# Performance work log

Measured on AMD Instinct MI355X. Metric: run time of the kernel, lower is better.

The kernel has to match this reference:

```python
import jax, jax.numpy as jnp
import numpy as np

MARGIN = 1.0

def setup_inputs() -> dict:
    key = jax.random.key(0)
    k1, k2, k3 = jax.random.split(key, 3)
    B, C, D = 65536, 1000, 512
    x = jax.random.normal(k1, (B, D), dtype=jnp.float32)
    x = x / jnp.linalg.norm(x, axis=1, keepdims=True)  # docstring: ||x||2 = 1
    labels = jax.random.randint(k2, (B,), 0, C, dtype=jnp.int64)
    centers = jax.random.normal(k3, (C, D), dtype=jnp.float32)
    return {"x": x, "labels": labels, "centers": centers}

def reference(x, labels, centers):
    # l2Norm applied to the centers (module is only used when l2Norm is truthy)
    c = centers / jnp.linalg.norm(centers, axis=1, keepdims=True)  # (C, D)
    # cosine distance to every center: one batched GEMM instead of per-sample loop
    dist = 1.0 - jnp.einsum("bd,cd->bc", x, c)                      # (B, C)
    pos = jnp.take_along_axis(dist, labels[:, None], axis=1)[:, 0]  # (B,)
    # min over all classes != label: mask own class with +inf
    same = jnp.arange(c.shape[0])[None, :] == labels[:, None]       # (B, C)
    neg = jnp.min(jnp.where(same, jnp.inf, dist), axis=1)           # (B,)
    # sum of per-sample hinge losses divided by batch size == mean
    return jnp.mean(jax.nn.relu(pos + MARGIN - neg))
```

## Files before the change

### kernel.cpp

```cpp
#include <hip/hip_runtime.h>
#include <stdint.h>

typedef short v8s __attribute__((ext_vector_type(8)));
typedef short v4s __attribute__((ext_vector_type(4)));
typedef float v4f __attribute__((ext_vector_type(4)));

#define BM 256
#define BN 128
#define BK 64
#define POS_INF __builtin_inff()

typedef __attribute__((address_space(3))) unsigned int lds_uint;
typedef const __attribute__((address_space(1))) unsigned int glb_uint;

__device__ __forceinline__ void load16_lds(const void* g, void* l) {
    __builtin_amdgcn_global_load_lds((glb_uint*)g, (lds_uint*)l, 16, 0, 0);
}

__device__ __forceinline__ short f2bf(float f) {
    uint32_t u = __builtin_bit_cast(uint32_t, f);
    u += 0x7fffu + ((u >> 16) & 1u);
    return (short)(u >> 16);
}

__global__ void prep(const float* __restrict__ centers,
                     unsigned short* __restrict__ cbf,
                     int C, int D, int CP, int CB,
                     const float* __restrict__ x,
                     unsigned short* __restrict__ xbf, size_t nx,
                     int* __restrict__ cnt, int NB,
                     float* __restrict__ out) {
    const int b = blockIdx.x;
    const int t = threadIdx.x;
    if (b == 0 && t == 0) out[0] = 0.0f;
    if (b < CB) {
        const int g = b * 256 + t;
        if (g < NB) cnt[g] = 0;
        const int wave = t >> 6, lane = t & 63;
        const int row = b * 4 + wave;
        if (row >= CP) return;
        if (row >= C) {
            v4s z = {0, 0, 0, 0};
            for (int d = lane * 4; d < D; d += 256)
                *(v4s*)&cbf[(size_t)row * D + d] = z;
            return;
        }
        const float* src = centers + (size_t)row * D;
        float ss = 0.0f;
        for (int d = lane * 4; d < D; d += 256) {
            v4f f = *(const v4f*)&src[d];
            ss += f.x * f.x + f.y * f.y + f.z * f.z + f.w * f.w;
        }
        #pragma unroll
        for (int off = 32; off; off >>= 1) ss += __shfl_xor(ss, off, 64);
        const float rn = rsqrtf(ss);
        for (int d = lane * 4; d < D; d += 256) {
            v4f f = *(const v4f*)&src[d];
            v4s s;
            s.x = f2bf(f.x * rn); s.y = f2bf(f.y * rn);
            s.z = f2bf(f.z * rn); s.w = f2bf(f.w * rn);
            *(v4s*)&cbf[(size_t)row * D + d] = s;
        }
    } else {
        const size_t i = ((size_t)(b - CB) * 256 + t) * 8;
        if (i >= nx) return;
        v4f f0 = *(const v4f*)&x[i];
        v4f f1 = *(const v4f*)&x[i + 4];
        v8s s;
        s[0] = f2bf(f0.x); s[1] = f2bf(f0.y); s[2] = f2bf(f0.z); s[3] = f2bf(f0.w);
        s[4] = f2bf(f1.x); s[5] = f2bf(f1.y); s[6] = f2bf(f1.z); s[7] = f2bf(f1.w);
        *(v8s*)&xbf[i] = s;
    }
}

__global__ void __launch_bounds__(512)
gemm_fused(const unsigned short* __restrict__ xbf,
           const unsigned short* __restrict__ cbf,
           const int* __restrict__ labels,
           float* __restrict__ pos, float* __restrict__ partial,
           int* __restrict__ cnt,
           int Bt, int C, int D, int NT, float margin,
           float* __restrict__ out) {
    __shared__ short LDSbuf[(BM + BN) * BK];
    short* As = LDSbuf;
    short* Bs = LDSbuf + BM * BK;

    const int t   = threadIdx.x;
    const int bid = blockIdx.x;
    const int xcd = bid & 7;
    const int per = bid >> 3;
    const int rowblk = (per >> 3) * 8 + xcd;
    const int nt     = per & 7;
    const int row0 = rowblk * BM;
    const int n0   = nt * BN;

    const int lane = t & 63;
    const int wave = t >> 6;
    const int wm = wave >> 1;
    const int wn = wave & 1;
    const int l15 = lane & 15, q = lane >> 4;

    const int rsub = lane >> 3;
    const int csrc = (lane & 7) ^ rsub;

    int myLab = 0;
    if (t < BM) myLab = labels[row0 + t];

    v4f acc[4][4];
    #pragma unroll
    for (int i = 0; i < 4; ++i)
        #pragma unroll
        for (int j = 0; j < 4; ++j)
            acc[i][j] = (v4f){0.f, 0.f, 0.f, 0.f};

    const int KT = D / BK;
    for (int kk = 0; kk < KT; ++kk) {
        const int k0 = kk * BK;
        #pragma unroll
        for (int p = 0; p < 4; ++p) {
            const int rbase = wave * 32 + p * 8;
            const unsigned short* g =
                &xbf[(size_t)(row0 + rbase + rsub) * D + k0 + csrc * 8];
            load16_lds(g, &As[rbase * BK]);
        }
        #pragma unroll
        for (int p = 0; p < 2; ++p) {
            const int rbase = wave * 16 + p * 8;
            const unsigned short* g =
                &cbf[(size_t)(n0 + rbase + rsub) * D + k0 + csrc * 8];
            load16_lds(g, &Bs[rbase * BK]);
        }
        __syncthreads();
        #pragma unroll
        for (int ki = 0; ki < BK; ki += 32) {
            const int cbase = ki >> 3;
            v8s a[4], b[4];
            #pragma unroll
            for (int i = 0; i < 4; ++i) {
                const int m = wm * 64 + i * 16 + l15;
                a[i] = *(const v8s*)&As[m * BK + (((cbase + q) ^ (l15 & 7)) * 8)];
            }
            #pragma unroll
            for (int j = 0; j < 4; ++j) {
                const int n = wn * 64 + j * 16 + l15;
                b[j] = *(const v8s*)&Bs[n * BK + (((cbase + q) ^ (l15 & 7)) * 8)];
            }
            #pragma unroll
            for (int i = 0; i < 4; ++i)
                #pragma unroll
                for (int j = 0; j < 4; ++j)
                    acc[i][j] = __builtin_amdgcn_mfma_f32_16x16x32_bf16(
                        a[i], b[j], acc[i][j], 0, 0, 0);
        }
        __syncthreads();
    }

    int*   Ls    = (int*)As;
    float* sMinW = (float*)Bs;
    int*   sLast = (int*)(Bs + 2 * BM * 2);
    float* wsum  = (float*)(sLast + 1);
    if (t < BM) Ls[t] = myLab;
    __syncthreads();

    #pragma unroll
    for (int i = 0; i < 4; ++i) {
        #pragma unroll
        for (int rg = 0; rg < 4; ++rg) {
            const int row_l = wm * 64 + i * 16 + q * 4 + rg;
            const int lab = Ls[row_l];
            float m = POS_INF;
            #pragma unroll
            for (int j = 0; j < 4; ++j) {
                const int col = n0 + wn * 64 + j * 16 + l15;
                const float d = 1.0f - acc[i][j][rg];
                if (col == lab)
                    __hip_atomic_store(&pos[row0 + row_l], d,
                                       __ATOMIC_RELAXED, __HIP_MEMORY_SCOPE_AGENT);
                else if (col < C) m = fminf(m, d);
            }
            m = fminf(m, __shfl_xor(m, 1, 64));
            m = fminf(m, __shfl_xor(m, 2, 64));
            m = fminf(m, __shfl_xor(m, 4, 64));
            m = fminf(m, __shfl_xor(m, 8, 64));
            if (l15 == 0) sMinW[wn * BM + row_l] = m;
        }
    }
    __syncthreads();
    if (t < BM) {
        const float m = fminf(sMinW[t], sMinW[BM + t]);
        __hip_atomic_store(&partial[(size_t)nt * Bt + row0 + t], m,
                           __ATOMIC_RELAXED, __HIP_MEMORY_SCOPE_AGENT);
    }
    __syncthreads();

    if (t == 0) {
        __builtin_amdgcn_s_waitcnt(0);
        const int old = __hip_atomic_fetch_add(&cnt[rowblk], 1,
                                               __ATOMIC_RELAXED,
                                               __HIP_MEMORY_SCOPE_AGENT);
        *sLast = (old == NT - 1);
    }
    __syncthreads();
    if (!*sLast) return;

    float hng = 0.0f;
    if (t < BM) {
        const int r = row0 + t;
        float neg = POS_INF;
        for (int tt = 0; tt < NT; ++tt)
            neg = fminf(neg, __hip_atomic_load(&partial[(size_t)tt * Bt + r],
                                               __ATOMIC_RELAXED,
                                               __HIP_MEMORY_SCOPE_AGENT));
        const float p = __hip_atomic_load(&pos[r], __ATOMIC_RELAXED,
                                          __HIP_MEMORY_SCOPE_AGENT);
        hng = fmaxf(0.0f, p + margin - neg);
    }
    #pragma unroll
    for (int off = 32; off; off >>= 1) hng += __shfl_down(hng, off, 64);
    if (lane == 0) wsum[wave] = hng;
    __syncthreads();
    if (t == 0) {
        float s = 0.0f;
        #pragma unroll
        for (int w = 0; w < 8; ++w) s += wsum[w];
        atomicAdd(out, s * (1.0f / (float)Bt));
    }
}

extern "C" void kernel_launch(void* const* d_in, const int* in_sizes, int n_in,
                              void* d_out, int out_size, void* d_ws, size_t ws_size,
                              hipStream_t stream) {
    const float* x       = (const float*)d_in[0];
    const int*   labels  = (const int*)d_in[1];
    const float* centers = (const float*)d_in[2];
    float* out = (float*)d_out;

    const int Bt = in_sizes[1];
    const int D  = in_sizes[0] / Bt;
    const int C  = in_sizes[2] / D;
    const int NT = (C + BN - 1) / BN;
    const int CP = NT * BN;
    const int NB = Bt / BM;

    char* ws = (char*)d_ws;
    unsigned short* cbf = (unsigned short*)ws;
    size_t off = (size_t)CP * D * 2;
    off = (off + 255) & ~(size_t)255;
    float* pos = (float*)(ws + off);      off += (size_t)Bt * 4;
    float* partial = (float*)(ws + off);  off += (size_t)NT * Bt * 4;
    int* cnt = (int*)(ws + off);          off += (size_t)NB * 4;
    off = (off + 255) & ~(size_t)255;
    unsigned short* xbf = (unsigned short*)(ws + off);

    const size_t nx = (size_t)Bt * D;
    const int CB = CP / 4;
    const int XB = (int)((nx / 8 + 255) / 256);
    prep<<<CB + XB, 256, 0, stream>>>(centers, cbf, C, D, CP, CB, x, xbf, nx,
                                      cnt, NB, out);

    gemm_fused<<<NB * NT, 512, 0, stream>>>(xbf, cbf, labels, pos, partial, cnt,
                                            Bt, C, D, NT, 1.0f, out);
}
```

Measured before the change: 283.1 us.

## Double-buffer LDS with interleaved async staging and 256x256 tiles

Widens the column tile from 128 to 256 so each block covers 4 center tiles instead of 8. Each wave now accumulates a 128x64 sub-tile, which raises arithmetic intensity per LDS read. The K loop uses two LDS buffers: global-to-LDS loads for the next K step are issued between the MFMA phases of the current step, with explicit vmcnt waits, barriers and setprio around the MFMAs. This is meant to hide global load latency and the per-iteration syncthreads stalls, at the cost of 128KB of dynamic LDS, more accumulator registers and a launch_bounds occupancy hint of 2.

After: 306.9 us. +8.4%, slower.

```diff
diff --git a/kernel.cpp b/kernel.cpp
--- a/kernel.cpp
+++ b/kernel.cpp
@@ -6,8 +6,11 @@
 typedef float v4f __attribute__((ext_vector_type(4)));
 
 #define BM 256
-#define BN 128
+#define BN 256
 #define BK 64
+#define ASH (BM * BK)
+#define BSH (BN * BK)
+#define BUFSH (ASH + BSH)
 #define POS_INF __builtin_inff()
 
 typedef __attribute__((address_space(3))) unsigned int lds_uint;
@@ -73,7 +76,50 @@
     }
 }
 
-__global__ void __launch_bounds__(512)
+#define BARRIER0() do { __builtin_amdgcn_s_barrier(); \
+                        __builtin_amdgcn_sched_barrier(0); } while (0)
+#define WAITVM(N)  do { asm volatile("s_waitcnt vmcnt(" #N ")" ::: "memory"); \
+                        __builtin_amdgcn_sched_barrier(0); } while (0)
+
+#define STAGE_A(dst, s, k0) \
+    load16_lds(&xbf[gA + (size_t)(s) * 32 * D + (size_t)(k0)], \
+               (dst) + ((s) * 32 + ((wave & 3) << 3) + ((wave >> 2) << 7)) * BK)
+#define STAGE_B(dst, bslot, k0) \
+    load16_lds(&cbf[gB + (size_t)(bslot) * 8 * D + (size_t)(k0)], \
+               (dst) + (wave * 32 + (bslot) * 8) * BK)
+
+#define LDS_A(Ac, p) do { \
+    _Pragma("unroll") \
+    for (int ii = 0; ii < 2; ++ii) { \
+        const int m_ = wm * 128 + (2 * (p) + ii) * 16 + l15; \
+        _Pragma("unroll") \
+        for (int kh = 0; kh < 2; ++kh) \
+            a[ii][kh] = *(const v8s*)&(Ac)[m_ * BK + ((((kh << 2) + q) ^ (l15 & 7)) << 3)]; \
+    } } while (0)
+
+#define LDS_B(Bc) do { \
+    _Pragma("unroll") \
+    for (int j = 0; j < 4; ++j) { \
+        const int n_ = wn * 64 + j * 16 + l15; \
+        _Pragma("unroll") \
+        for (int kh = 0; kh < 2; ++kh) \
+            b[j][kh] = *(const v8s*)&(Bc)[n_ * BK + ((((kh << 2) + q) ^ (l15 & 7)) << 3)]; \
+    } } while (0)
+
+#define MFMA16(p) do { \
+    __builtin_amdgcn_s_setprio(1); \
+    _Pragma("unroll") \
+    for (int ii = 0; ii < 2; ++ii) \
+        _Pragma("unroll") \
+        for (int j = 0; j < 4; ++j) \
+            _Pragma("unroll") \
+            for (int kh = 0; kh < 2; ++kh) \
+                acc[2 * (p) + ii][j] = __builtin_amdgcn_mfma_f32_16x16x32_bf16( \
+                    a[ii][kh], b[j][kh], acc[2 * (p) + ii][j], 0, 0, 0); \
+    __builtin_amdgcn_s_setprio(0); \
+} while (0)
+
+__global__ void __launch_bounds__(512, 2)
 gemm_fused(const unsigned short* __restrict__ xbf,
            const unsigned short* __restrict__ cbf,
            const int* __restrict__ labels,
@@ -81,92 +127,90 @@
            int* __restrict__ cnt,
            int Bt, int C, int D, int NT, float margin,
            float* __restrict__ out) {
-    __shared__ short LDSbuf[(BM + BN) * BK];
-    short* As = LDSbuf;
-    short* Bs = LDSbuf + BM * BK;
+    extern __shared__ short LDS[];
 
     const int t   = threadIdx.x;
     const int bid = blockIdx.x;
     const int xcd = bid & 7;
     const int per = bid >> 3;
-    const int rowblk = (per >> 3) * 8 + xcd;
-    const int nt     = per & 7;
+    const int rowblk = (per >> 2) * 8 + xcd;
+    const int nt     = per & 3;
     const int row0 = rowblk * BM;
     const int n0   = nt * BN;
 
     const int lane = t & 63;
     const int wave = t >> 6;
-    const int wm = wave >> 1;
-    const int wn = wave & 1;
+    const int wm = wave >> 2;
+    const int wn = wave & 3;
     const int l15 = lane & 15, q = lane >> 4;
-
     const int rsub = lane >> 3;
     const int csrc = (lane & 7) ^ rsub;
 
     int myLab = 0;
     if (t < BM) myLab = labels[row0 + t];
 
-    v4f acc[4][4];
+    const size_t gA = (size_t)(row0 + ((wave & 3) << 3) + ((wave >> 2) << 7) + rsub) * D + csrc * 8;
+    const size_t gB = (size_t)(n0 + wave * 32 + rsub) * D + csrc * 8;
+
+    v4f acc[8][4];
     #pragma unroll
-    for (int i = 0; i < 4; ++i)
+    for (int i = 0; i < 8; ++i)
         #pragma unroll
         for (int j = 0; j < 4; ++j)
             acc[i][j] = (v4f){0.f, 0.f, 0.f, 0.f};
 
     const int KT = D / BK;
-    for (int kk = 0; kk < KT; ++kk) {
-        const int k0 = kk * BK;
-        #pragma unroll
-        for (int p = 0; p < 4; ++p) {
-            const int rbase = wave * 32 + p * 8;
-            const unsigned short* g =
-                &xbf[(size_t)(row0 + rbase + rsub) * D + k0 + csrc * 8];
-            load16_lds(g, &As[rbase * BK]);
-        }
-        #pragma unroll
-        for (int p = 0; p < 2; ++p) {
-            const int rbase = wave * 16 + p * 8;
-            const unsigned short* g =
-                &cbf[(size_t)(n0 + rbase + rsub) * D + k0 + csrc * 8];
-            load16_lds(g, &Bs[rbase * BK]);
-        }
-        __syncthreads();
-        #pragma unroll
-        for (int ki = 0; ki < BK; ki += 32) {
-            const int cbase = ki >> 3;
-            v8s a[4], b[4];
-            #pragma unroll
-            for (int i = 0; i < 4; ++i) {
-                const int m = wm * 64 + i * 16 + l15;
-                a[i] = *(const v8s*)&As[m * BK + (((cbase + q) ^ (l15 & 7)) * 8)];
-            }
-            #pragma unroll
-            for (int j = 0; j < 4; ++j) {
-                const int n = wn * 64 + j * 16 + l15;
-                b[j] = *(const v8s*)&Bs[n * BK + (((cbase + q) ^ (l15 & 7)) * 8)];
-            }
-            #pragma unroll
-            for (int i = 0; i < 4; ++i)
-                #pragma unroll
-                for (int j = 0; j < 4; ++j)
-                    acc[i][j] = __builtin_amdgcn_mfma_f32_16x16x32_bf16(
-                        a[i], b[j], acc[i][j], 0, 0, 0);
-        }
-        __syncthreads();
-    }
-
-    int*   Ls    = (int*)As;
-    float* sMinW = (float*)Bs;
-    int*   sLast = (int*)(Bs + 2 * BM * 2);
-    float* wsum  = (float*)(sLast + 1);
+    v8s a[2][2], b[4][2];
+
+    {
+        short* An = LDS;  short* Bn = LDS + ASH;
+        STAGE_B(Bn, 0, 0); STAGE_B(Bn, 1, 0); STAGE_B(Bn, 2, 0); STAGE_B(Bn, 3, 0);
+        STAGE_A(An, 0, 0); STAGE_A(An, 1, 0); STAGE_A(An, 2, 0); STAGE_A(An, 3, 0);
+        WAITVM(3);
+        BARRIER0();
+    }
+
+    for (int kt = 0; kt < KT - 1; ++kt) {
+        short* Ac = LDS + (kt & 1) * BUFSH;        short* Bc = Ac + ASH;
+        short* An = LDS + ((kt & 1) ^ 1) * BUFSH;  short* Bn = An + ASH;
+        const int kn = (kt + 1) * BK;
+        LDS_B(Bc); LDS_A(Ac, 0);
+        STAGE_B(Bn, 0, kn); STAGE_B(Bn, 1, kn); STAGE_B(Bn, 2, kn);
+        BARRIER0(); MFMA16(0); WAITVM(5); BARRIER0();
+        LDS_A(Ac, 1);
+        STAGE_B(Bn, 3, kn); STAGE_A(An, 0, kn); STAGE_A(An, 1, kn);
+        BARRIER0(); MFMA16(1); WAITVM(7); BARRIER0();
+        LDS_A(Ac, 2);
+        STAGE_A(An, 2, kn); STAGE_A(An, 3, kn);
+        BARRIER0(); MFMA16(2); WAITVM(8); BARRIER0();
+        LDS_A(Ac, 3);
+        BARRIER0(); MFMA16(3); WAITVM(3); BARRIER0();
+    }
+    {
+        short* Ac = LDS + ((KT - 1) & 1) * BUFSH;  short* Bc = Ac + ASH;
+        LDS_B(Bc); LDS_A(Ac, 0);
+        BARRIER0(); MFMA16(0); WAITVM(2); BARRIER0();
+        LDS_A(Ac, 1);
+        BARRIER0(); MFMA16(1); WAITVM(1); BARRIER0();
+        LDS_A(Ac, 2);
+        BARRIER0(); MFMA16(2); WAITVM(0); BARRIER0();
+        LDS_A(Ac, 3);
+        BARRIER0(); MFMA16(3);
+    }
+    __syncthreads();
+
+    int*   Ls    = (int*)LDS;
+    float* sMinW = (float*)((char*)LDS + 1024);
+    int*   sLast = (int*)((char*)LDS + 5120);
+    float* wsum  = (float*)((char*)LDS + 5136);
     if (t < BM) Ls[t] = myLab;
     __syncthreads();
 
     #pragma unroll
-    for (int i = 0; i < 4; ++i) {
+    for (int i = 0; i < 8; ++i) {
         #pragma unroll
         for (int rg = 0; rg < 4; ++rg) {
-            const int row_l = wm * 64 + i * 16 + q * 4 + rg;
+            const int row_l = wm * 128 + i * 16 + q * 4 + rg;
             const int lab = Ls[row_l];
             float m = POS_INF;
             #pragma unroll
@@ -187,7 +231,8 @@
     }
     __syncthreads();
     if (t < BM) {
-        const float m = fminf(sMinW[t], sMinW[BM + t]);
+        const float m = fminf(fminf(sMinW[t], sMinW[BM + t]),
+                              fminf(sMinW[2 * BM + t], sMinW[3 * BM + t]));
         __hip_atomic_store(&partial[(size_t)nt * Bt + row0 + t], m,
                            __ATOMIC_RELAXED, __HIP_MEMORY_SCOPE_AGENT);
     }
@@ -258,6 +303,13 @@
     prep<<<CB + XB, 256, 0, stream>>>(centers, cbf, C, D, CP, CB, x, xbf, nx,
                                       cnt, NB, out);
 
-    gemm_fused<<<NB * NT, 512, 0, stream>>>(xbf, cbf, labels, pos, partial, cnt,
-                                            Bt, C, D, NT, 1.0f, out);
-}
+    static bool lds_attr_set = false;
+    if (!lds_attr_set) {
+        hipFuncSetAttribute(reinterpret_cast<const void*>(gemm_fused),
+                            hipFuncAttributeMaxDynamicSharedMemorySize,
+                            2 * BUFSH * (int)sizeof(short));
+        lds_attr_set = true;
+    }
+    gemm_fused<<<NB * NT, 512, 2 * BUFSH * sizeof(short), stream>>>(
+        xbf, cbf, labels, pos, partial, cnt, Bt, C, D, NT, 1.0f, out);
+}
```

## Load A fragments directly from global, double-buffer center tiles in LDS

Applied to the files above, without the earlier changes.

The A operand (x rows) is no longer staged through LDS. Each lane reads its MFMA fragments straight from global memory. Only the center tile goes to LDS, now double-buffered so the next K-tile loads while the current one is computed, with one barrier per iteration. This cuts LDS traffic and lowers LDS use for occupancy, but the uncoalesced 16-byte global reads of x rows may raise memory latency, and the x tile is no longer shared between the two waves that use it.

Result: slower. 415.5 us (+46.7%).

```diff
diff --git a/kernel.cpp b/kernel.cpp
--- a/kernel.cpp
+++ b/kernel.cpp
@@ -8,6 +8,7 @@
 #define BM 256
 #define BN 128
 #define BK 64
+#define BSH (BN * BK)
 #define POS_INF __builtin_inff()
 
 typedef __attribute__((address_space(3))) unsigned int lds_uint;
@@ -81,9 +82,7 @@
            int* __restrict__ cnt,
            int Bt, int C, int D, int NT, float margin,
            float* __restrict__ out) {
-    __shared__ short LDSbuf[(BM + BN) * BK];
-    short* As = LDSbuf;
-    short* Bs = LDSbuf + BM * BK;
+    __shared__ short Bsbuf[2 * BSH];
 
     const int t   = threadIdx.x;
     const int bid = blockIdx.x;
@@ -106,6 +105,8 @@
     int myLab = 0;
     if (t < BM) myLab = labels[row0 + t];
 
+    const unsigned short* gAl = xbf + (size_t)(row0 + wm * 64 + l15) * D + q * 8;
+
     v4f acc[4][4];
     #pragma unroll
     for (int i = 0; i < 4; ++i)
@@ -114,51 +115,57 @@
             acc[i][j] = (v4f){0.f, 0.f, 0.f, 0.f};
 
     const int KT = D / BK;
-    for (int kk = 0; kk < KT; ++kk) {
-        const int k0 = kk * BK;
-        #pragma unroll
-        for (int p = 0; p < 4; ++p) {
-            const int rbase = wave * 32 + p * 8;
-            const unsigned short* g =
-                &xbf[(size_t)(row0 + rbase + rsub) * D + k0 + csrc * 8];
-            load16_lds(g, &As[rbase * BK]);
-        }
-        #pragma unroll
-        for (int p = 0; p < 2; ++p) {
-            const int rbase = wave * 16 + p * 8;
-            const unsigned short* g =
-                &cbf[(size_t)(n0 + rbase + rsub) * D + k0 + csrc * 8];
-            load16_lds(g, &Bs[rbase * BK]);
-        }
-        __syncthreads();
-        #pragma unroll
-        for (int ki = 0; ki < BK; ki += 32) {
-            const int cbase = ki >> 3;
-            v8s a[4], b[4];
-            #pragma unroll
-            for (int i = 0; i < 4; ++i) {
-                const int m = wm * 64 + i * 16 + l15;
-                a[i] = *(const v8s*)&As[m * BK + (((cbase + q) ^ (l15 & 7)) * 8)];
+
+    #pragma unroll
+    for (int p = 0; p < 2; ++p) {
+        const int rbase = wave * 16 + p * 8;
+        load16_lds(&cbf[(size_t)(n0 + rbase + rsub) * D + csrc * 8],
+                   &Bsbuf[rbase * BK]);
+    }
+    __syncthreads();
+
+    for (int kt = 0; kt < KT; ++kt) {
+        const int k0 = kt * BK;
+        const short* Bc = Bsbuf + (kt & 1) * BSH;
+        short*       Bn = Bsbuf + ((kt & 1) ^ 1) * BSH;
+
+        v8s b[4][2];
+        #pragma unroll
+        for (int j = 0; j < 4; ++j) {
+            const int n = wn * 64 + j * 16 + l15;
+            #pragma unroll
+            for (int kh = 0; kh < 2; ++kh)
+                b[j][kh] = *(const v8s*)&Bc[n * BK + ((((kh << 2) + q) ^ (l15 & 7)) << 3)];
+        }
+        v8s a[4][2];
+        #pragma unroll
+        for (int i = 0; i < 4; ++i)
+            #pragma unroll
+            for (int kh = 0; kh < 2; ++kh)
+                a[i][kh] = *(const v8s*)&gAl[(size_t)i * 16 * D + k0 + kh * 32];
+        if (kt + 1 < KT) {
+            #pragma unroll
+            for (int p = 0; p < 2; ++p) {
+                const int rbase = wave * 16 + p * 8;
+                load16_lds(&cbf[(size_t)(n0 + rbase + rsub) * D + (k0 + BK) + csrc * 8],
+                           &Bn[rbase * BK]);
             }
-            #pragma unroll
-            for (int j = 0; j < 4; ++j) {
-                const int n = wn * 64 + j * 16 + l15;
-                b[j] = *(const v8s*)&Bs[n * BK + (((cbase + q) ^ (l15 & 7)) * 8)];
-            }
+        }
+        #pragma unroll
+        for (int kh = 0; kh < 2; ++kh)
             #pragma unroll
             for (int i = 0; i < 4; ++i)
                 #pragma unroll
                 for (int j = 0; j < 4; ++j)
                     acc[i][j] = __builtin_amdgcn_mfma_f32_16x16x32_bf16(
-                        a[i], b[j], acc[i][j], 0, 0, 0);
-        }
+                        a[i][kh], b[j][kh], acc[i][j], 0, 0, 0);
         __syncthreads();
     }
 
-    int*   Ls    = (int*)As;
-    float* sMinW = (float*)Bs;
-    int*   sLast = (int*)(Bs + 2 * BM * 2);
-    float* wsum  = (float*)(sLast + 1);
+    int*   Ls    = (int*)Bsbuf;
+    float* sMinW = (float*)((char*)Bsbuf + 1024);
+    int*   sLast = (int*)((char*)Bsbuf + 3072);
+    float* wsum  = (float*)((char*)Bsbuf + 3088);
     if (t < BM) Ls[t] = myLab;
     __syncthreads();
 
```

## Double-buffer LDS tiles with half-depth K stages to overlap loads and MFMA

Applied to the files above, without the earlier changes.

Splits the K=64 tile into two 32-wide stages held in two LDS buffers, issuing the global-to-LDS load for the next stage before computing on the current one. This is meant to hide global load latency behind MFMA work instead of serializing load, barrier and compute each iteration. The swizzle changes to a 4-chunk XOR pattern for 32-wide rows, and the epilogue scratch offsets are rewritten. The cost is twice as many barriers per K and a smaller swizzle, which may add LDS bank conflicts.

Result: slower. 291.9 us (+3.1%).

```diff
diff --git a/kernel.cpp b/kernel.cpp
--- a/kernel.cpp
+++ b/kernel.cpp
@@ -7,7 +7,8 @@
 
 #define BM 256
 #define BN 128
-#define BK 64
+#define BKH 32
+#define TSH ((BM + BN) * BKH)
 #define POS_INF __builtin_inff()
 
 typedef __attribute__((address_space(3))) unsigned int lds_uint;
@@ -81,9 +82,11 @@
            int* __restrict__ cnt,
            int Bt, int C, int D, int NT, float margin,
            float* __restrict__ out) {
-    __shared__ short LDSbuf[(BM + BN) * BK];
-    short* As = LDSbuf;
-    short* Bs = LDSbuf + BM * BK;
+    __shared__ short LDSbuf[2 * TSH];
+    short* As0 = LDSbuf;
+    short* Bs0 = LDSbuf + BM * BKH;
+    short* As1 = LDSbuf + TSH;
+    short* Bs1 = As1 + BM * BKH;
 
     const int t   = threadIdx.x;
     const int bid = blockIdx.x;
@@ -100,8 +103,8 @@
     const int wn = wave & 1;
     const int l15 = lane & 15, q = lane >> 4;
 
-    const int rsub = lane >> 3;
-    const int csrc = (lane & 7) ^ rsub;
+    const int rsub = lane >> 2;
+    const int csrc = (lane & 3) ^ (rsub & 3);
 
     int myLab = 0;
     if (t < BM) myLab = labels[row0 + t];
@@ -113,52 +116,54 @@
         for (int j = 0; j < 4; ++j)
             acc[i][j] = (v4f){0.f, 0.f, 0.f, 0.f};
 
-    const int KT = D / BK;
-    for (int kk = 0; kk < KT; ++kk) {
-        const int k0 = kk * BK;
-        #pragma unroll
-        for (int p = 0; p < 4; ++p) {
-            const int rbase = wave * 32 + p * 8;
-            const unsigned short* g =
-                &xbf[(size_t)(row0 + rbase + rsub) * D + k0 + csrc * 8];
-            load16_lds(g, &As[rbase * BK]);
-        }
-        #pragma unroll
-        for (int p = 0; p < 2; ++p) {
-            const int rbase = wave * 16 + p * 8;
-            const unsigned short* g =
-                &cbf[(size_t)(n0 + rbase + rsub) * D + k0 + csrc * 8];
-            load16_lds(g, &Bs[rbase * BK]);
-        }
+    #define STAGE(As_, Bs_, k0_) do {                                        \
+        load16_lds(&xbf[(size_t)(row0 + wave * 32 + rsub) * D + (k0_) + csrc * 8], \
+                   &(As_)[(wave * 32) * BKH]);                               \
+        load16_lds(&xbf[(size_t)(row0 + wave * 32 + 16 + rsub) * D + (k0_) + csrc * 8], \
+                   &(As_)[(wave * 32 + 16) * BKH]);                          \
+        load16_lds(&cbf[(size_t)(n0 + wave * 16 + rsub) * D + (k0_) + csrc * 8], \
+                   &(Bs_)[(wave * 16) * BKH]);                               \
+    } while (0)
+
+    #define TILE(As_, Bs_) do {                                              \
+        v8s a[4], b[4];                                                      \
+        _Pragma("unroll")                                                    \
+        for (int i = 0; i < 4; ++i)                                          \
+            a[i] = *(const v8s*)&(As_)[(wm * 64 + i * 16 + l15) * BKH        \
+                                       + ((q ^ (l15 & 3)) << 3)];            \
+        _Pragma("unroll")                                                    \
+        for (int j = 0; j < 4; ++j)                                          \
+            b[j] = *(const v8s*)&(Bs_)[(wn * 64 + j * 16 + l15) * BKH        \
+                                       + ((q ^ (l15 & 3)) << 3)];            \
+        _Pragma("unroll")                                                    \
+        for (int i = 0; i < 4; ++i)                                          \
+            _Pragma("unroll")                                                \
+            for (int j = 0; j < 4; ++j)                                      \
+                acc[i][j] = __builtin_amdgcn_mfma_f32_16x16x32_bf16(         \
+                    a[i], b[j], acc[i][j], 0, 0, 0);                         \
+    } while (0)
+
+    STAGE(As0, Bs0, 0);
+    __syncthreads();
+
+    const int KT2 = D / (2 * BKH);
+    for (int kt2 = 0; kt2 < KT2; ++kt2) {
+        const int k0 = kt2 * 64;
+        STAGE(As1, Bs1, k0 + 32);
+        TILE(As0, Bs0);
         __syncthreads();
-        #pragma unroll
-        for (int ki = 0; ki < BK; ki += 32) {
-            const int cbase = ki >> 3;
-            v8s a[4], b[4];
-            #pragma unroll
-            for (int i = 0; i < 4; ++i) {
-                const int m = wm * 64 + i * 16 + l15;
-                a[i] = *(const v8s*)&As[m * BK + (((cbase + q) ^ (l15 & 7)) * 8)];
-            }
-            #pragma unroll
-            for (int j = 0; j < 4; ++j) {
-                const int n = wn * 64 + j * 16 + l15;
-                b[j] = *(const v8s*)&Bs[n * BK + (((cbase + q) ^ (l15 & 7)) * 8)];
-            }
-            #pragma unroll
-            for (int i = 0; i < 4; ++i)
-                #pragma unroll
-                for (int j = 0; j < 4; ++j)
-                    acc[i][j] = __builtin_amdgcn_mfma_f32_16x16x32_bf16(
-                        a[i], b[j], acc[i][j], 0, 0, 0);
-        }
+        if (kt2 + 1 < KT2) STAGE(As0, Bs0, k0 + 64);
+        TILE(As1, Bs1);
         __syncthreads();
     }
 
-    int*   Ls    = (int*)As;
-    float* sMinW = (float*)Bs;
-    int*   sLast = (int*)(Bs + 2 * BM * 2);
-    float* wsum  = (float*)(sLast + 1);
+    #undef STAGE
+    #undef TILE
+
+    int*   Ls    = (int*)LDSbuf;
+    float* sMinW = (float*)((char*)LDSbuf + 1024);
+    int*   sLast = (int*)((char*)LDSbuf + 3072);
+    float* wsum  = (float*)((char*)LDSbuf + 3088);
     if (t < BM) Ls[t] = myLab;
     __syncthreads();
 
```
